# Performance work log

Hardware: AMD Instinct MI355X
Metric: run time of the kernel (lower is better)

The kernel has to match this reference:

```python
import jax, jax.numpy as jnp
import numpy as np
from jax import lax

H = W = 496
K = 5            # gabor kernel size
WIN = 16         # window_size
STRIDE = 16
PATCH = 32
GAMMA = 0.5
PSI = np.pi / 2
THETAS = np.array([np.pi/8, np.pi/4, 3*np.pi/8, np.pi/2, 5*np.pi/8, 6*np.pi/8, 7*np.pi/8, np.pi], dtype=np.float32)


def setup_inputs() -> dict:
    key = jax.random.key(0)
    k1, k2, k3 = jax.random.split(key, 3)
    img = jax.random.normal(k1, (1, 1, H, W), dtype=jnp.float32)
    sigmas = jax.random.uniform(k2, (1, 3), dtype=jnp.float32) * 10.0   # nn.Parameter(rand*10)
    lambdas = jax.random.uniform(k3, (1, 3), dtype=jnp.float32) * np.pi  # nn.Parameter(rand*pi)
    return {"img": img, "sigmas": sigmas, "lambdas": lambdas}


def _gabor_bank(sigmas, lambdas):
    # axes: (sigma, lambda, theta, ky, kx)
    idx = jnp.arange(K, dtype=jnp.float32) - (K - 1) / 2.0
    sig = sigmas[0][:, None, None, None, None]          # [3,1,1,1,1]
    lam = lambdas[0][None, :, None, None, None]         # [1,3,1,1,1]
    th = jnp.asarray(THETAS)[None, None, :, None, None] # [1,1,8,1,1]
    y = idx[None, None, None, :, None]
    x = idx[None, None, None, None, :]
    sigma_x = sig
    sigma_y = sig / GAMMA
    sin_t, cos_t = jnp.sin(th), jnp.cos(th)
    y_theta = -x * sin_t + y * cos_t
    x_theta = x * cos_t + y * sin_t
    gb = jnp.exp(-0.5 * (x_theta**2 / sigma_x**2 + y_theta**2 / sigma_y**2)) \
         * jnp.cos(2.0 * np.pi * x_theta / lam + PSI)
    return gb.reshape(-1, 1, K, K)  # [72,1,5,5]


def reference(img, sigmas, lambdas):
    gb = _gabor_bank(sigmas, lambdas)
    res = lax.conv_general_dilated(
        img, gb, window_strides=(1, 1), padding=[(K // 2, K // 2)] * 2,
        dimension_numbers=("NCHW", "OIHW", "NCHW"))          # [1,72,H,W]
    res = res.reshape(1, 9, 8, H, W).max(axis=2)              # max over 8 thetas -> [1,9,H,W]
    out = res[0]                                              # [9,H,W]

    # find_maxima: per-channel threshold at 5*mean, zero below (torch.nn.Threshold)
    mean = out.mean(axis=(1, 2), keepdims=True)
    thr = jnp.where(out > mean * 5.0, out, 0.0)

    nw = H // STRIDE                                          # 31
    windows = thr.reshape(9, nw, WIN, nw, WIN).transpose(0, 1, 3, 2, 4).reshape(9, nw * nw, WIN * WIN)
    is_max = jnp.argmax(windows, axis=2) == (WIN * WIN) // 2  # [9, 961]

    w_idx = jnp.arange(nw * nw)
    rows = w_idx // nw * STRIDE + WIN // 2
    cols = w_idx % nw * STRIDE + WIN // 2

    # describe: zero-pad by 16, gather 32x32 patch at each candidate keypoint for every channel
    pad = jnp.pad(out, ((0, 0), (16, 16), (16, 16)))
    pr = rows[:, None, None] + jnp.arange(PATCH)[None, :, None]   # [961,32,1]
    pc = cols[:, None, None] + jnp.arange(PATCH)[None, None, :]   # [961,1,32]
    patches = pad[:, pr, pc]                                      # [9,961,32,32]

    # keep patches only for detected keypoints with nonzero content (original skips zero patches)
    valid_kp = jnp.any(is_max, axis=0)                            # [961]
    nonzero = jnp.any(patches != 0, axis=(2, 3))                  # [9,961]
    mask = (valid_kp[None, :] & nonzero).astype(patches.dtype)
    patches = patches * mask[:, :, None, None]
    return patches
```

## Files before the change

### kernel.cpp

```cpp
#include <hip/hip_runtime.h>
#include <math.h>

#define HH 496
#define WW 496
#define HWSZ (HH*WW)
#define NW 31
#define NWIN (NW*NW)

typedef float nf4 __attribute__((ext_vector_type(4)));

__constant__ float c_thetas[8] = {
    0.39269908169872414f, 0.7853981633974483f, 1.1780972450961724f,
    1.5707963267948966f,  1.9634954084936207f, 2.356194490192345f,
    2.748893571891069f,   3.141592653589793f};

__global__ void bank_kernel(const float* __restrict__ sigmas,
                            const float* __restrict__ lambdas,
                            float* __restrict__ filt,
                            float* __restrict__ meanacc) {
    int idx = threadIdx.x + blockIdx.x * blockDim.x;
    if (idx >= 1800) {
        if (idx < 1809) meanacc[(idx - 1800) * 16] = 0.0f;
        return;
    }
    int f = idx / 25, k = idx % 25;
    int dy = k / 5, dx = k % 5;
    int s = f / 24, rem = f % 24, l = rem / 8, t = rem % 8;
    float sig = sigmas[s], lam = lambdas[l], th = c_thetas[t];
    float y = (float)dy - 2.0f, x = (float)dx - 2.0f;
    float st = sinf(th), ct = cosf(th);
    float yt = -x * st + y * ct;
    float xt =  x * ct + y * st;
    float sx2 = sig * sig;
    float sy2 = 4.0f * sig * sig;
    float g = expf(-0.5f * (xt * xt / sx2 + yt * yt / sy2)) *
              cosf(6.28318530717958647692f * xt / lam + 1.5707963267948966f);
    filt[k * 72 + f] = g;
}

#define FMAS(FP, P) \
    a0  = fmaf(P, (FP)[0],  a0);  a1  = fmaf(P, (FP)[1],  a1);  \
    a2  = fmaf(P, (FP)[2],  a2);  a3  = fmaf(P, (FP)[3],  a3);  \
    a4  = fmaf(P, (FP)[4],  a4);  a5  = fmaf(P, (FP)[5],  a5);  \
    a6  = fmaf(P, (FP)[6],  a6);  a7  = fmaf(P, (FP)[7],  a7);  \
    a8  = fmaf(P, (FP)[8],  a8);  a9  = fmaf(P, (FP)[9],  a9);  \
    a10 = fmaf(P, (FP)[10], a10); a11 = fmaf(P, (FP)[11], a11); \
    a12 = fmaf(P, (FP)[12], a12); a13 = fmaf(P, (FP)[13], a13); \
    a14 = fmaf(P, (FP)[14], a14); a15 = fmaf(P, (FP)[15], a15); \
    a16 = fmaf(P, (FP)[16], a16); a17 = fmaf(P, (FP)[17], a17); \
    a18 = fmaf(P, (FP)[18], a18); a19 = fmaf(P, (FP)[19], a19); \
    a20 = fmaf(P, (FP)[20], a20); a21 = fmaf(P, (FP)[21], a21); \
    a22 = fmaf(P, (FP)[22], a22); a23 = fmaf(P, (FP)[23], a23);

#define STEP(K) { const float* fp = fbase + (K)*72; FMAS(fp, p##K) }

#define ALLSTEPS \
    STEP(0)  STEP(1)  STEP(2)  STEP(3)  STEP(4)  \
    STEP(5)  STEP(6)  STEP(7)  STEP(8)  STEP(9)  \
    STEP(10) STEP(11) STEP(12) STEP(13) STEP(14) \
    STEP(15) STEP(16) STEP(17) STEP(18) STEP(19) \
    STEP(20) STEP(21) STEP(22) STEP(23) STEP(24)

#define RED(CC, MV) { \
        float s = MV; \
        s += __shfl_down(s, 32, 64); s += __shfl_down(s, 16, 64); \
        s += __shfl_down(s,  8, 64); s += __shfl_down(s,  4, 64); \
        s += __shfl_down(s,  2, 64); s += __shfl_down(s,  1, 64); \
        if ((tid & 63) == 0) red[tid >> 6][CC] = s; }

#define CONVCG(CG) { \
        float a0=0,a1=0,a2=0,a3=0,a4=0,a5=0,a6=0,a7=0,a8=0,a9=0,a10=0,a11=0, \
              a12=0,a13=0,a14=0,a15=0,a16=0,a17=0,a18=0,a19=0,a20=0,a21=0,a22=0,a23=0; \
        const float* fbase = filt + (CG) * 24; \
        ALLSTEPS \
        float m0 = fmaxf(fmaxf(fmaxf(a0,a1),fmaxf(a2,a3)),fmaxf(fmaxf(a4,a5),fmaxf(a6,a7))); \
        float m1 = fmaxf(fmaxf(fmaxf(a8,a9),fmaxf(a10,a11)),fmaxf(fmaxf(a12,a13),fmaxf(a14,a15))); \
        float m2 = fmaxf(fmaxf(fmaxf(a16,a17),fmaxf(a18,a19)),fmaxf(fmaxf(a20,a21),fmaxf(a22,a23))); \
        out[((CG) * 3 + 0) * HWSZ + y * WW + x] = m0; \
        out[((CG) * 3 + 1) * HWSZ + y * WW + x] = m1; \
        out[((CG) * 3 + 2) * HWSZ + y * WW + x] = m2; \
        RED((CG) * 3 + 0, m0) RED((CG) * 3 + 1, m1) RED((CG) * 3 + 2, m2) \
    }

__global__ __launch_bounds__(256) void conv_kernel(
    const float* __restrict__ img, const float* __restrict__ filt,
    float* __restrict__ out, float* __restrict__ meanacc) {
    __shared__ float tile[20 * 20];
    __shared__ float red[4][9];
    int tid = threadIdx.x;
    int tx = tid & 15, ty = tid >> 4;
    int bx = blockIdx.x, by = blockIdx.y;

    for (int i = tid; i < 400; i += 256) {
        int tY = i / 20, tX = i % 20;
        int gy = by * 16 + tY - 2, gx = bx * 16 + tX - 2;
        float v = 0.0f;
        if (gy >= 0 && gy < HH && gx >= 0 && gx < WW) v = img[gy * WW + gx];
        tile[i] = v;
    }
    __syncthreads();

    int tbase = ty * 20 + tx;
    float p0  = tile[tbase +  0], p1  = tile[tbase +  1], p2  = tile[tbase +  2],
          p3  = tile[tbase +  3], p4  = tile[tbase +  4];
    float p5  = tile[tbase + 20], p6  = tile[tbase + 21], p7  = tile[tbase + 22],
          p8  = tile[tbase + 23], p9  = tile[tbase + 24];
    float p10 = tile[tbase + 40], p11 = tile[tbase + 41], p12 = tile[tbase + 42],
          p13 = tile[tbase + 43], p14 = tile[tbase + 44];
    float p15 = tile[tbase + 60], p16 = tile[tbase + 61], p17 = tile[tbase + 62],
          p18 = tile[tbase + 63], p19 = tile[tbase + 64];
    float p20 = tile[tbase + 80], p21 = tile[tbase + 81], p22 = tile[tbase + 82],
          p23 = tile[tbase + 83], p24 = tile[tbase + 84];

    int y = by * 16 + ty, x = bx * 16 + tx;

    CONVCG(0)
    CONVCG(1)
    CONVCG(2)

    __syncthreads();
    if (tid < 9)
        atomicAdd(&meanacc[tid * 16],
                  red[0][tid] + red[1][tid] + red[2][tid] + red[3][tid]);
}

__global__ __launch_bounds__(256) void patch_kernel(
    const float* __restrict__ out, const float* __restrict__ meanacc,
    float* __restrict__ dst) {
    int w = blockIdx.x;
    int r = w / NW, cl = w % NW;
    int tid = threadIdx.x;
    __shared__ int lds_and[4];
    __shared__ int lds_or[4];

    int wy = tid >> 4, wx = tid & 15;
    int rowbase = (r * 16 + wy) * WW + cl * 16 + wx;
    int cbase   = (r * 16 + 8) * WW + cl * 16;
    int okmask = 0;
#pragma unroll
    for (int c = 0; c < 9; c++) {
        float m5 = meanacc[c * 16] * (5.0f / (float)HWSZ);
        float v  = out[c * HWSZ + rowbase];
        float vc = out[c * HWSZ + cbase];
        float thr  = (v  > m5) ? v  : 0.0f;
        float thrc = (vc > m5) ? vc : 0.0f;
        bool ok = (tid < 128) ? (thr < thrc) : (thr <= thrc);
        okmask |= (ok ? 1 : 0) << c;
    }
#pragma unroll
    for (int off = 1; off < 64; off <<= 1) okmask &= __shfl_xor(okmask, off, 64);
    if ((tid & 63) == 0) lds_and[tid >> 6] = okmask;
    __syncthreads();

    int am = lds_and[0] & lds_and[1] & lds_and[2] & lds_and[3];

    int i = tid >> 3;
    int jg = (tid & 7) << 2;
    size_t dbase = (size_t)w * 1024 + i * 32 + jg;

    if (am == 0) {
        nf4 z = (nf4){0.f, 0.f, 0.f, 0.f};
#pragma unroll
        for (int c = 0; c < 9; c++)
            __builtin_nontemporal_store(z, (nf4*)(dst + (size_t)c * NWIN * 1024 + dbase));
        return;
    }

    int row = r * 16 + i - 8;
    int col = cl * 16 + jg - 8;
    bool inb = (row >= 0 && row < HH && col >= 0 && col + 3 < WW);
    size_t pbase = (size_t)row * WW + col;
    int nzmask = 0;
    nf4 p0, p1, p2, p3, p4, p5, p6, p7, p8;
#define LOADP(C, V) { \
        V = (nf4){0.f, 0.f, 0.f, 0.f}; \
        if (inb) V = *(const nf4*)(out + (size_t)(C) * HWSZ + pbase); \
        if (V.x != 0.f || V.y != 0.f || V.z != 0.f || V.w != 0.f) nzmask |= 1 << (C); }
    LOADP(0,p0) LOADP(1,p1) LOADP(2,p2) LOADP(3,p3) LOADP(4,p4)
    LOADP(5,p5) LOADP(6,p6) LOADP(7,p7) LOADP(8,p8)

#pragma unroll
    for (int off = 1; off < 64; off <<= 1) nzmask |= __shfl_xor(nzmask, off, 64);
    if ((tid & 63) == 0) lds_or[tid >> 6] = nzmask;
    __syncthreads();

    int om = lds_or[0] | lds_or[1] | lds_or[2] | lds_or[3];

#define STOREP(C, V) { \
        float mk = ((om >> (C)) & 1) ? 1.0f : 0.0f; \
        V *= mk; \
        __builtin_nontemporal_store(V, (nf4*)(dst + (size_t)(C) * NWIN * 1024 + dbase)); }
    STOREP(0,p0) STOREP(1,p1) STOREP(2,p2) STOREP(3,p3) STOREP(4,p4)
    STOREP(5,p5) STOREP(6,p6) STOREP(7,p7) STOREP(8,p8)
}

extern "C" void kernel_launch(void* const* d_in, const int* in_sizes, int n_in,
                              void* d_out, int out_size, void* d_ws, size_t ws_size,
                              hipStream_t stream) {
    const float* img     = (const float*)d_in[0];
    const float* sigmas  = (const float*)d_in[1];
    const float* lambdas = (const float*)d_in[2];
    float* ws = (float*)d_ws;
    float* filt    = ws;
    float* meanacc = ws + 2048;
    float* outb    = ws + 4096;

    bank_kernel<<<8, 256, 0, stream>>>(sigmas, lambdas, filt, meanacc);
    conv_kernel<<<dim3(NW, NW), 256, 0, stream>>>(img, filt, outb, meanacc);
    patch_kernel<<<NWIN, 256, 0, stream>>>(outb, meanacc, (float*)d_out);
}
```

Before: 120.9 us.

## Fuse Gabor bank into conv kernel, replace atomic mean with per-block partials

Drops the separate bank kernel: every conv block now computes all 1800 Gabor filter taps into LDS and reads the filters from LDS instead of global memory. The global atomicAdd for channel sums is replaced by per-block partial sums, which every patch block then reduces itself (9x961 reads per block). This removes one launch and the atomics and the need to zero the accumulator, but adds redundant transcendental work in every conv block and a redundant reduction in every patch block.

```diff
diff --git a/kernel.cpp b/kernel.cpp
--- a/kernel.cpp
+++ b/kernel.cpp
@@ -6,6 +6,7 @@
 #define HWSZ (HH*WW)
 #define NW 31
 #define NWIN (NW*NW)
+#define PARTSTRIDE 1024
 
 typedef float nf4 __attribute__((ext_vector_type(4)));
 
@@ -14,52 +15,28 @@
     1.5707963267948966f,  1.9634954084936207f, 2.356194490192345f,
     2.748893571891069f,   3.141592653589793f};
 
-__global__ void bank_kernel(const float* __restrict__ sigmas,
-                            const float* __restrict__ lambdas,
-                            float* __restrict__ filt,
-                            float* __restrict__ meanacc) {
-    int idx = threadIdx.x + blockIdx.x * blockDim.x;
-    if (idx >= 1800) {
-        if (idx < 1809) meanacc[(idx - 1800) * 16] = 0.0f;
-        return;
-    }
-    int f = idx / 25, k = idx % 25;
-    int dy = k / 5, dx = k % 5;
-    int s = f / 24, rem = f % 24, l = rem / 8, t = rem % 8;
-    float sig = sigmas[s], lam = lambdas[l], th = c_thetas[t];
-    float y = (float)dy - 2.0f, x = (float)dx - 2.0f;
-    float st = sinf(th), ct = cosf(th);
-    float yt = -x * st + y * ct;
-    float xt =  x * ct + y * st;
-    float sx2 = sig * sig;
-    float sy2 = 4.0f * sig * sig;
-    float g = expf(-0.5f * (xt * xt / sx2 + yt * yt / sy2)) *
-              cosf(6.28318530717958647692f * xt / lam + 1.5707963267948966f);
-    filt[k * 72 + f] = g;
-}
-
-#define FMAS(FP, P) \
-    a0  = fmaf(P, (FP)[0],  a0);  a1  = fmaf(P, (FP)[1],  a1);  \
-    a2  = fmaf(P, (FP)[2],  a2);  a3  = fmaf(P, (FP)[3],  a3);  \
-    a4  = fmaf(P, (FP)[4],  a4);  a5  = fmaf(P, (FP)[5],  a5);  \
-    a6  = fmaf(P, (FP)[6],  a6);  a7  = fmaf(P, (FP)[7],  a7);  \
-    a8  = fmaf(P, (FP)[8],  a8);  a9  = fmaf(P, (FP)[9],  a9);  \
-    a10 = fmaf(P, (FP)[10], a10); a11 = fmaf(P, (FP)[11], a11); \
-    a12 = fmaf(P, (FP)[12], a12); a13 = fmaf(P, (FP)[13], a13); \
-    a14 = fmaf(P, (FP)[14], a14); a15 = fmaf(P, (FP)[15], a15); \
-    a16 = fmaf(P, (FP)[16], a16); a17 = fmaf(P, (FP)[17], a17); \
-    a18 = fmaf(P, (FP)[18], a18); a19 = fmaf(P, (FP)[19], a19); \
-    a20 = fmaf(P, (FP)[20], a20); a21 = fmaf(P, (FP)[21], a21); \
-    a22 = fmaf(P, (FP)[22], a22); a23 = fmaf(P, (FP)[23], a23);
-
-#define STEP(K) { const float* fp = fbase + (K)*72; FMAS(fp, p##K) }
-
-#define ALLSTEPS \
-    STEP(0)  STEP(1)  STEP(2)  STEP(3)  STEP(4)  \
-    STEP(5)  STEP(6)  STEP(7)  STEP(8)  STEP(9)  \
-    STEP(10) STEP(11) STEP(12) STEP(13) STEP(14) \
-    STEP(15) STEP(16) STEP(17) STEP(18) STEP(19) \
-    STEP(20) STEP(21) STEP(22) STEP(23) STEP(24)
+#define FMAS(B, P) \
+    a0  = fmaf(P, flds[(B)+0],  a0);  a1  = fmaf(P, flds[(B)+1],  a1);  \
+    a2  = fmaf(P, flds[(B)+2],  a2);  a3  = fmaf(P, flds[(B)+3],  a3);  \
+    a4  = fmaf(P, flds[(B)+4],  a4);  a5  = fmaf(P, flds[(B)+5],  a5);  \
+    a6  = fmaf(P, flds[(B)+6],  a6);  a7  = fmaf(P, flds[(B)+7],  a7);  \
+    a8  = fmaf(P, flds[(B)+8],  a8);  a9  = fmaf(P, flds[(B)+9],  a9);  \
+    a10 = fmaf(P, flds[(B)+10], a10); a11 = fmaf(P, flds[(B)+11], a11); \
+    a12 = fmaf(P, flds[(B)+12], a12); a13 = fmaf(P, flds[(B)+13], a13); \
+    a14 = fmaf(P, flds[(B)+14], a14); a15 = fmaf(P, flds[(B)+15], a15); \
+    a16 = fmaf(P, flds[(B)+16], a16); a17 = fmaf(P, flds[(B)+17], a17); \
+    a18 = fmaf(P, flds[(B)+18], a18); a19 = fmaf(P, flds[(B)+19], a19); \
+    a20 = fmaf(P, flds[(B)+20], a20); a21 = fmaf(P, flds[(B)+21], a21); \
+    a22 = fmaf(P, flds[(B)+22], a22); a23 = fmaf(P, flds[(B)+23], a23);
+
+#define STEP(K, CG) { FMAS((K)*72 + (CG)*24, p##K) }
+
+#define ALLSTEPS(CG) \
+    STEP(0,CG)  STEP(1,CG)  STEP(2,CG)  STEP(3,CG)  STEP(4,CG)  \
+    STEP(5,CG)  STEP(6,CG)  STEP(7,CG)  STEP(8,CG)  STEP(9,CG)  \
+    STEP(10,CG) STEP(11,CG) STEP(12,CG) STEP(13,CG) STEP(14,CG) \
+    STEP(15,CG) STEP(16,CG) STEP(17,CG) STEP(18,CG) STEP(19,CG) \
+    STEP(20,CG) STEP(21,CG) STEP(22,CG) STEP(23,CG) STEP(24,CG)
 
 #define RED(CC, MV) { \
         float s = MV; \
@@ -71,8 +48,7 @@
 #define CONVCG(CG) { \
         float a0=0,a1=0,a2=0,a3=0,a4=0,a5=0,a6=0,a7=0,a8=0,a9=0,a10=0,a11=0, \
               a12=0,a13=0,a14=0,a15=0,a16=0,a17=0,a18=0,a19=0,a20=0,a21=0,a22=0,a23=0; \
-        const float* fbase = filt + (CG) * 24; \
-        ALLSTEPS \
+        ALLSTEPS(CG) \
         float m0 = fmaxf(fmaxf(fmaxf(a0,a1),fmaxf(a2,a3)),fmaxf(fmaxf(a4,a5),fmaxf(a6,a7))); \
         float m1 = fmaxf(fmaxf(fmaxf(a8,a9),fmaxf(a10,a11)),fmaxf(fmaxf(a12,a13),fmaxf(a14,a15))); \
         float m2 = fmaxf(fmaxf(fmaxf(a16,a17),fmaxf(a18,a19)),fmaxf(fmaxf(a20,a21),fmaxf(a22,a23))); \
@@ -83,9 +59,11 @@
     }
 
 __global__ __launch_bounds__(256) void conv_kernel(
-    const float* __restrict__ img, const float* __restrict__ filt,
-    float* __restrict__ out, float* __restrict__ meanacc) {
+    const float* __restrict__ img,
+    const float* __restrict__ sigmas, const float* __restrict__ lambdas,
+    float* __restrict__ out, float* __restrict__ partial) {
     __shared__ float tile[20 * 20];
+    __shared__ __align__(16) float flds[1800];
     __shared__ float red[4][9];
     int tid = threadIdx.x;
     int tx = tid & 15, ty = tid >> 4;
@@ -97,6 +75,21 @@
         float v = 0.0f;
         if (gy >= 0 && gy < HH && gx >= 0 && gx < WW) v = img[gy * WW + gx];
         tile[i] = v;
+    }
+    for (int idx = tid; idx < 1800; idx += 256) {
+        int f = idx / 25, k = idx % 25;
+        int dy = k / 5, dx = k % 5;
+        int s = f / 24, rem = f % 24, l = rem / 8, t = rem % 8;
+        float sig = sigmas[s], lam = lambdas[l], th = c_thetas[t];
+        float yy = (float)dy - 2.0f, xx = (float)dx - 2.0f;
+        float st = sinf(th), ct = cosf(th);
+        float yt = -xx * st + yy * ct;
+        float xt =  xx * ct + yy * st;
+        float sx2 = sig * sig;
+        float sy2 = 4.0f * sig * sig;
+        float g = expf(-0.5f * (xt * xt / sx2 + yt * yt / sy2)) *
+                  cosf(6.28318530717958647692f * xt / lam + 1.5707963267948966f);
+        flds[k * 72 + f] = g;
     }
     __syncthreads();
 
@@ -119,19 +112,35 @@
     CONVCG(2)
 
     __syncthreads();
-    if (tid < 9)
-        atomicAdd(&meanacc[tid * 16],
-                  red[0][tid] + red[1][tid] + red[2][tid] + red[3][tid]);
+    if (tid < 9) {
+        int bid = by * NW + bx;
+        partial[tid * PARTSTRIDE + bid] =
+            red[0][tid] + red[1][tid] + red[2][tid] + red[3][tid];
+    }
 }
 
 __global__ __launch_bounds__(256) void patch_kernel(
-    const float* __restrict__ out, const float* __restrict__ meanacc,
+    const float* __restrict__ out, const float* __restrict__ partial,
     float* __restrict__ dst) {
     int w = blockIdx.x;
     int r = w / NW, cl = w % NW;
     int tid = threadIdx.x;
+    __shared__ float sm5[9];
     __shared__ int lds_and[4];
     __shared__ int lds_or[4];
+
+    {
+        int lane = tid & 63, wid = tid >> 6;
+        for (int c = wid; c < 9; c += 4) {
+            float s = 0.0f;
+            for (int b = lane; b < NWIN; b += 64) s += partial[c * PARTSTRIDE + b];
+            s += __shfl_down(s, 32, 64); s += __shfl_down(s, 16, 64);
+            s += __shfl_down(s,  8, 64); s += __shfl_down(s,  4, 64);
+            s += __shfl_down(s,  2, 64); s += __shfl_down(s,  1, 64);
+            if (lane == 0) sm5[c] = s * (5.0f / (float)HWSZ);
+        }
+    }
+    __syncthreads();
 
     int wy = tid >> 4, wx = tid & 15;
     int rowbase = (r * 16 + wy) * WW + cl * 16 + wx;
@@ -139,7 +148,7 @@
     int okmask = 0;
 #pragma unroll
     for (int c = 0; c < 9; c++) {
-        float m5 = meanacc[c * 16] * (5.0f / (float)HWSZ);
+        float m5 = sm5[c];
         float v  = out[c * HWSZ + rowbase];
         float vc = out[c * HWSZ + cbase];
         float thr  = (v  > m5) ? v  : 0.0f;
@@ -201,11 +210,9 @@
     const float* sigmas  = (const float*)d_in[1];
     const float* lambdas = (const float*)d_in[2];
     float* ws = (float*)d_ws;
-    float* filt    = ws;
-    float* meanacc = ws + 2048;
-    float* outb    = ws + 4096;
-
-    bank_kernel<<<8, 256, 0, stream>>>(sigmas, lambdas, filt, meanacc);
-    conv_kernel<<<dim3(NW, NW), 256, 0, stream>>>(img, filt, outb, meanacc);
-    patch_kernel<<<NWIN, 256, 0, stream>>>(outb, meanacc, (float*)d_out);
+    float* partial = ws;
+    float* outb    = ws + 16384;
+
+    conv_kernel<<<dim3(NW, NW), 256, 0, stream>>>(img, sigmas, lambdas, outb, partial);
+    patch_kernel<<<NWIN, 256, 0, stream>>>(outb, partial, (float*)d_out);
 }
```

After: 119.0 us. No clear change (-1.6%).
